# Kernel optimization log

Measured on AMD Instinct MI355X. Metric: run time of the kernel, lower is better.

## Reference

```python
import jax, jax.numpy as jnp
import numpy as np

EPS = 1e-6
N = 512
D = 8192


def solve_lap_np(cost):
    """Jonker-Volgenant shortest-augmenting-path LAP (same optimum as
    scipy.optimize.linear_sum_assignment). Returns col4row: col assigned to each row."""
    cost = np.asarray(cost, dtype=np.float64)
    n = cost.shape[0]
    u = np.zeros(n)
    v = np.zeros(n)
    path = np.full(n, -1, dtype=np.int64)
    col4row = np.full(n, -1, dtype=np.int64)
    row4col = np.full(n, -1, dtype=np.int64)
    for cur_row in range(n):
        shortest = np.full(n, np.inf)
        SR = np.zeros(n, dtype=bool)  # visited rows
        SC = np.zeros(n, dtype=bool)  # visited cols
        i = cur_row
        min_val = 0.0
        sink = -1
        while sink == -1:
            SR[i] = True
            idx = np.nonzero(~SC)[0]
            r = min_val + cost[i, idx] - u[i] - v[idx]
            upd = r < shortest[idx]
            shortest[idx[upd]] = r[upd]
            path[idx[upd]] = i
            j = idx[np.argmin(shortest[idx])]
            min_val = shortest[j]
            SC[j] = True
            if row4col[j] == -1:
                sink = j
            else:
                i = row4col[j]
        # dual updates
        u[cur_row] += min_val
        sr = np.nonzero(SR)[0]
        sr = sr[sr != cur_row]
        u[sr] += min_val - shortest[col4row[sr]]
        sc = np.nonzero(SC)[0]
        v[sc] -= min_val - shortest[sc]
        # augment along the alternating path
        j = sink
        while True:
            i = path[j]
            row4col[j] = i
            col4row[i], j = j, col4row[i]
            if i == cur_row:
                break
    return col4row


def lap_assign(cost):
    """Optimal assignment as a one-hot labelling matrix (rows -> cols)."""
    n = cost.shape[0]
    col = jax.pure_callback(
        lambda c: solve_lap_np(np.asarray(c)).astype(np.int32),
        jax.ShapeDtypeStruct((n,), jnp.int32),
        cost,
    )
    return jax.nn.one_hot(col, n, dtype=cost.dtype)


def l2_normalize(x):
    # torch F.normalize(p=2, dim=1): x / max(||x||, eps)
    norm = jnp.sqrt(jnp.sum(x * x, axis=1, keepdims=True))
    return x / jnp.maximum(norm, EPS)


def setup_inputs() -> dict:
    key = jax.random.key(0)
    k1, k2, k3 = jax.random.split(key, 3)
    return {
        "un1": jax.random.normal(k1, (N, D), dtype=jnp.float32),
        "un2": jax.random.normal(k2, (N, D), dtype=jnp.float32),
        "un3": jax.random.normal(k3, (N, D), dtype=jnp.float32),
    }


def reference(un1, un2, un3):
    n1 = l2_normalize(un1)
    n2 = l2_normalize(un2)
    n3 = l2_normalize(un3)
    # cosine-distance cost matrices, cycle 1->2->3->1
    c12 = 1.0 - n1 @ n2.T
    c23 = 1.0 - n2 @ n3.T
    c31 = 1.0 - n3 @ n1.T
    x12 = lap_assign(c12)
    x23 = lap_assign(c23)
    x31 = lap_assign(c31)
    return (x12, x23, x31)
```

## Files before the change

kernel.cpp:

```cpp
#include <hip/hip_runtime.h>
#include <math.h>

#define NN 512
#define DD 8192

__global__ __launch_bounds__(256) void norm_kernel(
    const float* __restrict__ a0, const float* __restrict__ a1,
    const float* __restrict__ a2, float* __restrict__ scales) {
  const float* mats[3] = {a0, a1, a2};
  const int m = blockIdx.y;
  const int row = blockIdx.x;
  const float* x = mats[m] + (size_t)row * DD;
  const int tid = threadIdx.x;
  float s = 0.f;
  for (int k = tid * 4; k < DD; k += 256 * 4) {
    const float4 v = *(const float4*)(x + k);
    s += v.x * v.x + v.y * v.y + v.z * v.z + v.w * v.w;
  }
#pragma unroll
  for (int off = 32; off > 0; off >>= 1) s += __shfl_down(s, off);
  __shared__ float ws[4];
  if ((tid & 63) == 0) ws[tid >> 6] = s;
  __syncthreads();
  if (tid == 0) {
    const float t = ws[0] + ws[1] + ws[2] + ws[3];
    scales[m * NN + row] = 1.0f / fmaxf(sqrtf(t), 1e-6f);
  }
}

__global__ __launch_bounds__(256) void cost_gemm_kernel(
    const float* __restrict__ a0, const float* __restrict__ a1,
    const float* __restrict__ a2, const float* __restrict__ scales,
    float* __restrict__ cost_all) {
  const float* mats[3] = {a0, a1, a2};
  const int p = blockIdx.z;
  const int pA = p, pB = (p + 1) % 3;
  const float* A = mats[pA];
  const float* B = mats[pB];
  float* C = cost_all + (size_t)p * NN * NN;

  __shared__ float lds_a[32 * 64];
  __shared__ float lds_b[32 * 64];

  const int tid = threadIdx.x;
  const int rowBase = blockIdx.y * 64;
  const int colBase = blockIdx.x * 64;

  const int lr = tid & 63;
  const int lq = tid >> 6;

  const float* Arow = A + (size_t)(rowBase + lr) * DD;
  const float* Brow = B + (size_t)(colBase + lr) * DD;

  float acc[4][4];
#pragma unroll
  for (int i = 0; i < 4; ++i)
#pragma unroll
    for (int j = 0; j < 4; ++j) acc[i][j] = 0.f;

  const int tx = tid & 15, ty = tid >> 4;

  for (int kb = 0; kb < DD; kb += 32) {
#pragma unroll
    for (int qq = 0; qq < 2; ++qq) {
      const int q = lq + qq * 4;
      const float4 av = *(const float4*)(Arow + kb + q * 4);
      const float4 bv = *(const float4*)(Brow + kb + q * 4);
      lds_a[(q * 4 + 0) * 64 + lr] = av.x;
      lds_a[(q * 4 + 1) * 64 + lr] = av.y;
      lds_a[(q * 4 + 2) * 64 + lr] = av.z;
      lds_a[(q * 4 + 3) * 64 + lr] = av.w;
      lds_b[(q * 4 + 0) * 64 + lr] = bv.x;
      lds_b[(q * 4 + 1) * 64 + lr] = bv.y;
      lds_b[(q * 4 + 2) * 64 + lr] = bv.z;
      lds_b[(q * 4 + 3) * 64 + lr] = bv.w;
    }
    __syncthreads();
#pragma unroll
    for (int k = 0; k < 32; ++k) {
      const float4 a4 = *(const float4*)(&lds_a[k * 64 + ty * 4]);
      const float4 b4 = *(const float4*)(&lds_b[k * 64 + tx * 4]);
      const float as0[4] = {a4.x, a4.y, a4.z, a4.w};
      const float bs0[4] = {b4.x, b4.y, b4.z, b4.w};
#pragma unroll
      for (int ii = 0; ii < 4; ++ii)
#pragma unroll
        for (int jj = 0; jj < 4; ++jj)
          acc[ii][jj] = fmaf(as0[ii], bs0[jj], acc[ii][jj]);
    }
    __syncthreads();
  }

#pragma unroll
  for (int ii = 0; ii < 4; ++ii) {
    const int gr = rowBase + ty * 4 + ii;
    const float sa = scales[pA * NN + gr];
#pragma unroll
    for (int jj = 0; jj < 4; ++jj) {
      const int gc = colBase + tx * 4 + jj;
      const float sb = scales[pB * NN + gc];
      C[gr * NN + gc] = 1.0f - acc[ii][jj] * sa * sb;
    }
  }
}


__device__ __forceinline__ int SW(int c) { return ((c & 7) << 6) | (c >> 3); }

__device__ __forceinline__ unsigned wave_min_u32(unsigned x) {
  int t;
  t = __builtin_amdgcn_update_dpp((int)x, (int)x, 0x111, 0xf, 0xf, false);
  x = ((unsigned)t < x) ? (unsigned)t : x;
  t = __builtin_amdgcn_update_dpp((int)x, (int)x, 0x112, 0xf, 0xf, false);
  x = ((unsigned)t < x) ? (unsigned)t : x;
  t = __builtin_amdgcn_update_dpp((int)x, (int)x, 0x114, 0xf, 0xf, false);
  x = ((unsigned)t < x) ? (unsigned)t : x;
  t = __builtin_amdgcn_update_dpp((int)x, (int)x, 0x118, 0xf, 0xf, false);
  x = ((unsigned)t < x) ? (unsigned)t : x;
  t = __builtin_amdgcn_update_dpp((int)x, (int)x, 0x142, 0xf, 0xf, false);
  x = ((unsigned)t < x) ? (unsigned)t : x;
  t = __builtin_amdgcn_update_dpp((int)x, (int)x, 0x143, 0xf, 0xf, false);
  x = ((unsigned)t < x) ? (unsigned)t : x;
  return (unsigned)__builtin_amdgcn_readlane((int)x, 63);
}

__device__ __forceinline__ double readlane_f64(double x, int lane) {
  const long long b = __double_as_longlong(x);
  const int lo = __builtin_amdgcn_readlane((int)(b & 0xffffffffLL), lane);
  const int hi = __builtin_amdgcn_readlane((int)(b >> 32), lane);
  return __longlong_as_double(((long long)hi << 32) | (unsigned long long)(unsigned)lo);
}

__global__ __launch_bounds__(64) void lap_kernel(
    const float* __restrict__ cost_all, float* __restrict__ out) {
  const int p = blockIdx.x;
  const float* cost = cost_all + (size_t)p * NN * NN;
  float* outp = out + (size_t)p * NN * NN;
  const int tid = threadIdx.x;

  __shared__ double sh_u[NN];
  __shared__ double sh_shortest[NN];
  __shared__ int sh_path[NN];
  __shared__ int sh_col4row[NN];
  __shared__ int sh_row4col[NN];

  const double INF = __builtin_inf();

  for (int k = tid; k < NN; k += 64) {
    sh_u[k] = 0.0;
    sh_col4row[k] = -1;
    sh_row4col[k] = -1;
  }
  double myV[8];
#pragma unroll
  for (int q = 0; q < 8; ++q) myV[q] = 0.0;
  __syncthreads();

  for (int cur_row = 0; cur_row < NN; ++cur_row) {
    double selv[8];
    double vAdj[8];
    double frz[8];
    int myPath[8];
    unsigned pl[8];
#pragma unroll
    for (int q = 0; q < 8; ++q) {
      selv[q] = INF;
      vAdj[q] = myV[q];
      frz[q] = 0.0;
      myPath[q] = 0;
    }
#pragma unroll
    for (int q = 0; q < 8; ++q)
      pl[q] = ((unsigned)q << 10) | (unsigned)(sh_row4col[SW(tid * 8 + q)] + 1);

    unsigned scMask = 0, srMask = 0;
    int i = cur_row;
    double minv = 0.0;
    int sink = -1;
    int pendQ = -1, pendLane = 0;

    while (true) {
      if ((i >> 3) == tid) srMask |= 1u << (i & 7);
      const float4 c0 = *(const float4*)(cost + (size_t)i * NN + tid * 8);
      const float4 c1 = *(const float4*)(cost + (size_t)i * NN + tid * 8 + 4);
      const double u_i = sh_u[SW(i)];
      if (pendQ >= 0) {
        const bool me = (tid == pendLane);
#define APPLY_SC(K)                                                     \
        if (pendQ == K) {                                               \
          if (me) {                                                     \
            selv[K] = INF; vAdj[K] = -INF; frz[K] = minv;               \
            scMask |= 1u << K;                                          \
          }                                                             \
        }
        APPLY_SC(0) APPLY_SC(1) APPLY_SC(2) APPLY_SC(3)
        APPLY_SC(4) APPLY_SC(5) APPLY_SC(6) APPLY_SC(7)
#undef APPLY_SC
      }
      const float cf[8] = {c0.x, c0.y, c0.z, c0.w, c1.x, c1.y, c1.z, c1.w};
#pragma unroll
      for (int q = 0; q < 8; ++q) {
        const double r = ((minv + (double)cf[q]) - u_i) - vAdj[q];
        const bool cnd = r < selv[q];
        selv[q] = fmin(selv[q], r);
        myPath[q] = cnd ? i : myPath[q];
      }
      const bool t01 = selv[1] < selv[0];
      double v01 = t01 ? selv[1] : selv[0]; unsigned p01 = t01 ? pl[1] : pl[0];
      const bool t23 = selv[3] < selv[2];
      double v23 = t23 ? selv[3] : selv[2]; unsigned p23 = t23 ? pl[3] : pl[2];
      const bool t45 = selv[5] < selv[4];
      double v45 = t45 ? selv[5] : selv[4]; unsigned p45 = t45 ? pl[5] : pl[4];
      const bool t67 = selv[7] < selv[6];
      double v67 = t67 ? selv[7] : selv[6]; unsigned p67 = t67 ? pl[7] : pl[6];
      const bool ta = v23 < v01;
      const double vab = ta ? v23 : v01; const unsigned pab = ta ? p23 : p01;
      const bool tb = v67 < v45;
      const double vcd = tb ? v67 : v45; const unsigned pcd = tb ? p67 : p45;
      const bool tc = vcd < vab;
      const double lv = tc ? vcd : vab; const unsigned lp = tc ? pcd : pab;
      const long long bb = __double_as_longlong(lv);
      const unsigned long long kk =
          (bb < 0) ? ~(unsigned long long)bb
                   : ((unsigned long long)bb | 0x8000000000000000ULL);
      const unsigned hi = (unsigned)(kk >> 32);
      const unsigned lo = (unsigned)kk;
      const unsigned minhi = wave_min_u32(hi);
      unsigned long long bal = __ballot(hi == minhi);
      int srcLane;
      if (__popcll(bal) == 1) {
        srcLane = __ffsll(bal) - 1;
      } else {
        const unsigned lo2 = (hi == minhi) ? lo : 0xFFFFFFFFu;
        const unsigned minlo = wave_min_u32(lo2);
        bal = __ballot((hi == minhi) && (lo == minlo));
        srcLane = __ffsll(bal) - 1;
      }
      minv = readlane_f64(lv, srcLane);
      const unsigned pw = (unsigned)__builtin_amdgcn_readlane((int)lp, srcLane);
      const int qb = (int)(pw >> 10);
      const int r4 = (int)(pw & 0x3FFu) - 1;
      if (r4 < 0) {
        sink = srcLane * 8 + qb;
        break;
      }
      i = r4;
      pendQ = qb;
      pendLane = srcLane;
    }

#pragma unroll
    for (int q = 0; q < 8; ++q) {
      sh_shortest[SW(tid * 8 + q)] = frz[q];
      sh_path[SW(tid * 8 + q)] = myPath[q];
    }
    __syncthreads();
#pragma unroll
    for (int q = 0; q < 8; ++q) {
      const int row = tid * 8 + q;
      if (row == cur_row) {
        sh_u[SW(row)] += minv;
      } else if (srMask & (1u << q)) {
        sh_u[SW(row)] += minv - sh_shortest[SW(sh_col4row[SW(row)])];
      }
      if (scMask & (1u << q)) myV[q] -= minv - frz[q];
    }
    __syncthreads();
    if (tid == 0) {
      int j = sink;
      while (true) {
        const int pi = sh_path[SW(j)];
        sh_row4col[SW(j)] = pi;
        const int tmp = sh_col4row[SW(pi)];
        sh_col4row[SW(pi)] = j;
        j = tmp;
        if (pi == cur_row) break;
      }
    }
    __syncthreads();
  }

#pragma unroll
  for (int q = 0; q < 8; ++q) {
    const int row = tid * 8 + q;
    outp[(size_t)row * NN + sh_col4row[SW(row)]] = 1.0f;
  }
}

extern "C" void kernel_launch(void* const* d_in, const int* in_sizes, int n_in,
                              void* d_out, int out_size, void* d_ws, size_t ws_size,
                              hipStream_t stream) {
  const float* un1 = (const float*)d_in[0];
  const float* un2 = (const float*)d_in[1];
  const float* un3 = (const float*)d_in[2];
  float* out = (float*)d_out;

  float* cost = (float*)d_ws;
  float* scales = cost + (size_t)3 * NN * NN;

  hipMemsetAsync(d_out, 0, (size_t)out_size * sizeof(float), stream);

  norm_kernel<<<dim3(NN, 3), 256, 0, stream>>>(un1, un2, un3, scales);
  cost_gemm_kernel<<<dim3(NN / 64, NN / 64, 3), 256, 0, stream>>>(un1, un2, un3, scales, cost);
  lap_kernel<<<3, 64, 0, stream>>>(cost, out);
}
```

Before: 5.735 ms.

## Add JV column reduction, reduction transfer and augmenting row reduction before LAP

Adds the Jonker-Volgenant initialization phases (column reduction, reduction transfer, two passes of augmenting row reduction) so that most rows are assigned before the shortest-augmenting-path phase. The augmentation loop then runs only over the remaining free rows, with a guard on the Dijkstra loop. This is meant to cut the number of expensive serial augmentations that dominate the single-wave LAP kernel. The risk is that ties may give a different optimal assignment than the reference, and the extra serial work in the preprocessing phases adds cost.

```diff
diff --git a/kernel.cpp b/kernel.cpp
--- a/kernel.cpp
+++ b/kernel.cpp
@@ -131,6 +131,30 @@
   return __longlong_as_double(((long long)hi << 32) | (unsigned long long)(unsigned)lo);
 }
 
+__device__ __forceinline__ unsigned long long f64key(double x) {
+  const long long b = __double_as_longlong(x);
+  return (b < 0) ? ~(unsigned long long)b
+                 : ((unsigned long long)b | 0x8000000000000000ULL);
+}
+
+__device__ __forceinline__ int wave_argmin_f64(double x, double* mv) {
+  const unsigned long long k = f64key(x);
+  const unsigned hi = (unsigned)(k >> 32), lo = (unsigned)k;
+  const unsigned minhi = wave_min_u32(hi);
+  unsigned long long bal = __ballot(hi == minhi);
+  int lane;
+  if (__popcll(bal) == 1) {
+    lane = __ffsll(bal) - 1;
+  } else {
+    const unsigned lo2 = (hi == minhi) ? lo : 0xFFFFFFFFu;
+    const unsigned minlo = wave_min_u32(lo2);
+    bal = __ballot((hi == minhi) && (lo == minlo));
+    lane = __ffsll(bal) - 1;
+  }
+  *mv = readlane_f64(x, lane);
+  return lane;
+}
+
 __global__ __launch_bounds__(64) void lap_kernel(
     const float* __restrict__ cost_all, float* __restrict__ out) {
   const int p = blockIdx.x;
@@ -139,24 +163,170 @@
   const int tid = threadIdx.x;
 
   __shared__ double sh_u[NN];
+  __shared__ double sh_v[NN];
   __shared__ double sh_shortest[NN];
   __shared__ int sh_path[NN];
-  __shared__ int sh_col4row[NN];
-  __shared__ int sh_row4col[NN];
+  __shared__ int sh_x[NN];
+  __shared__ int sh_y[NN];
+  __shared__ int sh_cnt[NN];
+  __shared__ int sh_free[NN];
 
   const double INF = __builtin_inf();
 
-  for (int k = tid; k < NN; k += 64) {
-    sh_u[k] = 0.0;
-    sh_col4row[k] = -1;
-    sh_row4col[k] = -1;
-  }
+#pragma unroll
+  for (int q = 0; q < 8; ++q) {
+    const int e = tid * 8 + q;
+    sh_x[SW(e)] = -1;
+    sh_y[SW(e)] = -1;
+    sh_cnt[SW(e)] = 0;
+  }
+  __syncthreads();
+
+  float colv[8];
+  int imin[8];
+#pragma unroll
+  for (int q = 0; q < 8; ++q) { colv[q] = __builtin_inff(); imin[q] = 0; }
+  for (int i = 0; i < NN; i += 2) {
+    const float4 a0 = *(const float4*)(cost + (size_t)i * NN + tid * 8);
+    const float4 a1 = *(const float4*)(cost + (size_t)i * NN + tid * 8 + 4);
+    const float4 b0 = *(const float4*)(cost + (size_t)(i + 1) * NN + tid * 8);
+    const float4 b1 = *(const float4*)(cost + (size_t)(i + 1) * NN + tid * 8 + 4);
+    const float fa[8] = {a0.x, a0.y, a0.z, a0.w, a1.x, a1.y, a1.z, a1.w};
+    const float fb[8] = {b0.x, b0.y, b0.z, b0.w, b1.x, b1.y, b1.z, b1.w};
+#pragma unroll
+    for (int q = 0; q < 8; ++q) {
+      if (fa[q] < colv[q]) { colv[q] = fa[q]; imin[q] = i; }
+      if (fb[q] < colv[q]) { colv[q] = fb[q]; imin[q] = i + 1; }
+    }
+  }
+#pragma unroll
+  for (int q = 0; q < 8; ++q) {
+    sh_v[SW(tid * 8 + q)] = (double)colv[q];
+    atomicMax(&sh_x[SW(imin[q])], tid * 8 + q);
+    atomicAdd(&sh_cnt[SW(imin[q])], 1);
+  }
+  __syncthreads();
+#pragma unroll
+  for (int q = 0; q < 8; ++q) {
+    const int j = tid * 8 + q;
+    sh_y[SW(j)] = (sh_x[SW(imin[q])] == j) ? imin[q] : -1;
+  }
+  __syncthreads();
+
+  for (int q0 = 0; q0 < 8; ++q0) {
+    const bool rt = (sh_cnt[SW(tid * 8 + q0)] == 1);
+    unsigned long long mask = __ballot(rt);
+    while (mask) {
+      const int lane = __ffsll(mask) - 1;
+      mask &= mask - 1;
+      const int i = lane * 8 + q0;
+      const int j1 = sh_x[SW(i)];
+      const float4 c0 = *(const float4*)(cost + (size_t)i * NN + tid * 8);
+      const float4 c1 = *(const float4*)(cost + (size_t)i * NN + tid * 8 + 4);
+      const float cf[8] = {c0.x, c0.y, c0.z, c0.w, c1.x, c1.y, c1.z, c1.w};
+      double m = INF;
+#pragma unroll
+      for (int q = 0; q < 8; ++q) {
+        const int col = tid * 8 + q;
+        double h = (double)cf[q] - sh_v[SW(col)];
+        if (col == j1) h = INF;
+        m = fmin(m, h);
+      }
+      double gmin;
+      (void)wave_argmin_f64(m, &gmin);
+      if (tid == 0) sh_v[SW(j1)] = sh_v[SW(j1)] - gmin;
+    }
+  }
+  __syncthreads();
+
+  int numfree = 0;
+  for (int q0 = 0; q0 < 8; ++q0) {
+    const int row = tid * 8 + q0;
+    const bool fr = (sh_x[SW(row)] < 0);
+    const unsigned long long mask = __ballot(fr);
+    if (fr) {
+      const int pos = numfree + (int)__popcll(mask & ((1ull << tid) - 1ull));
+      sh_free[pos] = row;
+    }
+    numfree += (int)__popcll(mask);
+  }
+  __syncthreads();
+
+  int nf = numfree;
+  for (int pass = 0; pass < 2; ++pass) {
+    int k = 0;
+    const int prv = nf;
+    nf = 0;
+    int guard = 0;
+    while (k < prv && ++guard < 5000) {
+      const int i = sh_free[k];
+      k++;
+      const float4 c0 = *(const float4*)(cost + (size_t)i * NN + tid * 8);
+      const float4 c1 = *(const float4*)(cost + (size_t)i * NN + tid * 8 + 4);
+      const float cf[8] = {c0.x, c0.y, c0.z, c0.w, c1.x, c1.y, c1.z, c1.w};
+      double um = (double)cf[0] - sh_v[SW(tid * 8)];
+      int j1q = tid * 8;
+      double us = INF;
+      int j2q = tid * 8;
+#pragma unroll
+      for (int q = 1; q < 8; ++q) {
+        const double h = (double)cf[q] - sh_v[SW(tid * 8 + q)];
+        const int col = tid * 8 + q;
+        if (h < us) {
+          if (h >= um) { us = h; j2q = col; }
+          else { us = um; j2q = j1q; um = h; j1q = col; }
+        }
+      }
+      double g_umin;
+      const int lane1 = wave_argmin_f64(um, &g_umin);
+      const double su = (tid == lane1) ? us : um;
+      double g_usub;
+      const int lane2 = wave_argmin_f64(su, &g_usub);
+      int j1 = __builtin_amdgcn_readlane(j1q, lane1);
+      const int j2 = __builtin_amdgcn_readlane((lane2 == lane1) ? j2q : j1q, lane2);
+      int i0 = sh_y[SW(j1)];
+      const bool strict = g_umin < g_usub;
+      if (strict) {
+        if (tid == 0) sh_v[SW(j1)] = sh_v[SW(j1)] - (g_usub - g_umin);
+      } else if (i0 >= 0) {
+        j1 = j2;
+        i0 = sh_y[SW(j1)];
+      }
+      if (tid == 0) { sh_x[SW(i)] = j1; sh_y[SW(j1)] = i; }
+      if (i0 >= 0) {
+        if (strict) {
+          k--;
+          if (tid == 0) sh_free[k] = i0;
+        } else {
+          if (tid == 0) sh_free[nf] = i0;
+          nf++;
+        }
+      }
+    }
+    if (k < prv) {
+      for (int t = k; t < prv; ++t) {
+        if (tid == 0) sh_free[nf] = sh_free[t];
+        nf++;
+      }
+    }
+  }
+  __syncthreads();
+
   double myV[8];
 #pragma unroll
-  for (int q = 0; q < 8; ++q) myV[q] = 0.0;
-  __syncthreads();
-
-  for (int cur_row = 0; cur_row < NN; ++cur_row) {
+  for (int q = 0; q < 8; ++q) {
+    const int row = tid * 8 + q;
+    const int xr = sh_x[SW(row)];
+    double uu = 0.0;
+    if (xr >= 0) uu = (double)cost[(size_t)row * NN + xr] - sh_v[SW(xr)];
+    sh_u[SW(row)] = uu;
+    myV[q] = sh_v[SW(tid * 8 + q)];
+  }
+  __syncthreads();
+
+  for (int ff = 0; ff < nf; ++ff) {
+    const int cur_row = sh_free[ff];
+
     double selv[8];
     double vAdj[8];
     double frz[8];
@@ -171,15 +341,16 @@
     }
 #pragma unroll
     for (int q = 0; q < 8; ++q)
-      pl[q] = ((unsigned)q << 10) | (unsigned)(sh_row4col[SW(tid * 8 + q)] + 1);
+      pl[q] = ((unsigned)q << 10) | (unsigned)(sh_y[SW(tid * 8 + q)] + 1);
 
     unsigned scMask = 0, srMask = 0;
     int i = cur_row;
     double minv = 0.0;
     int sink = -1;
     int pendQ = -1, pendLane = 0;
-
-    while (true) {
+    int guard = 0;
+
+    while (++guard <= NN + 2) {
       if ((i >> 3) == tid) srMask |= 1u << (i & 7);
       const float4 c0 = *(const float4*)(cost + (size_t)i * NN + tid * 8);
       const float4 c1 = *(const float4*)(cost + (size_t)i * NN + tid * 8 + 4);
@@ -219,10 +390,7 @@
       const double vcd = tb ? v67 : v45; const unsigned pcd = tb ? p67 : p45;
       const bool tc = vcd < vab;
       const double lv = tc ? vcd : vab; const unsigned lp = tc ? pcd : pab;
-      const long long bb = __double_as_longlong(lv);
-      const unsigned long long kk =
-          (bb < 0) ? ~(unsigned long long)bb
-                   : ((unsigned long long)bb | 0x8000000000000000ULL);
+      const unsigned long long kk = f64key(lv);
       const unsigned hi = (unsigned)(kk >> 32);
       const unsigned lo = (unsigned)kk;
       const unsigned minhi = wave_min_u32(hi);
@@ -249,41 +417,43 @@
       pendLane = srcLane;
     }
 
-#pragma unroll
-    for (int q = 0; q < 8; ++q) {
-      sh_shortest[SW(tid * 8 + q)] = frz[q];
-      sh_path[SW(tid * 8 + q)] = myPath[q];
-    }
-    __syncthreads();
-#pragma unroll
-    for (int q = 0; q < 8; ++q) {
-      const int row = tid * 8 + q;
-      if (row == cur_row) {
-        sh_u[SW(row)] += minv;
-      } else if (srMask & (1u << q)) {
-        sh_u[SW(row)] += minv - sh_shortest[SW(sh_col4row[SW(row)])];
-      }
-      if (scMask & (1u << q)) myV[q] -= minv - frz[q];
-    }
-    __syncthreads();
-    if (tid == 0) {
-      int j = sink;
-      while (true) {
-        const int pi = sh_path[SW(j)];
-        sh_row4col[SW(j)] = pi;
-        const int tmp = sh_col4row[SW(pi)];
-        sh_col4row[SW(pi)] = j;
-        j = tmp;
-        if (pi == cur_row) break;
-      }
-    }
-    __syncthreads();
+    if (sink >= 0) {
+#pragma unroll
+      for (int q = 0; q < 8; ++q) {
+        sh_shortest[SW(tid * 8 + q)] = frz[q];
+        sh_path[SW(tid * 8 + q)] = myPath[q];
+      }
+      __syncthreads();
+#pragma unroll
+      for (int q = 0; q < 8; ++q) {
+        const int row = tid * 8 + q;
+        if (row == cur_row) {
+          sh_u[SW(row)] += minv;
+        } else if (srMask & (1u << q)) {
+          sh_u[SW(row)] += minv - sh_shortest[SW(sh_x[SW(row)])];
+        }
+        if (scMask & (1u << q)) myV[q] -= minv - frz[q];
+      }
+      __syncthreads();
+      if (tid == 0) {
+        int j = sink;
+        while (true) {
+          const int pi = sh_path[SW(j)];
+          sh_y[SW(j)] = pi;
+          const int tmp = sh_x[SW(pi)];
+          sh_x[SW(pi)] = j;
+          j = tmp;
+          if (pi == cur_row) break;
+        }
+      }
+      __syncthreads();
+    }
   }
 
 #pragma unroll
   for (int q = 0; q < 8; ++q) {
     const int row = tid * 8 + q;
-    outp[(size_t)row * NN + sh_col4row[SW(row)]] = 1.0f;
+    outp[(size_t)row * NN + sh_x[SW(row)]] = 1.0f;
   }
 }
 
```

Result: slower. 11.27 ms (+96.5%).

## Add JV column-reduction initialization to LAP so augmentation runs only for free rows

Applied to the files above, without the earlier changes.

Adds a Jonker-Volgenant style column reduction before augmentation. Each column's dual is set to its minimum cost, that minimum row is assigned when uncontested, and the free rows are compacted into a list so the shortest-augmenting-path phase only iterates over unassigned rows. It also precomputes minv-u_i-v per column to trim the inner double-precision arithmetic, and adds a loop guard. This aims to cut the number of serial Dijkstra augmentations, at the cost of a full cost-matrix scan and a risk of ties or degenerate cases yielding a different optimal assignment.

```diff
diff --git a/kernel.cpp b/kernel.cpp
--- a/kernel.cpp
+++ b/kernel.cpp
@@ -131,6 +131,12 @@
   return __longlong_as_double(((long long)hi << 32) | (unsigned long long)(unsigned)lo);
 }
 
+__device__ __forceinline__ unsigned long long f64key(double x) {
+  const long long b = __double_as_longlong(x);
+  return (b < 0) ? ~(unsigned long long)b
+                 : ((unsigned long long)b | 0x8000000000000000ULL);
+}
+
 __global__ __launch_bounds__(64) void lap_kernel(
     const float* __restrict__ cost_all, float* __restrict__ out) {
   const int p = blockIdx.x;
@@ -141,22 +147,67 @@
   __shared__ double sh_u[NN];
   __shared__ double sh_shortest[NN];
   __shared__ int sh_path[NN];
-  __shared__ int sh_col4row[NN];
-  __shared__ int sh_row4col[NN];
+  __shared__ int sh_x[NN];
+  __shared__ int sh_y[NN];
+  __shared__ int sh_free[NN];
 
   const double INF = __builtin_inf();
 
-  for (int k = tid; k < NN; k += 64) {
-    sh_u[k] = 0.0;
-    sh_col4row[k] = -1;
-    sh_row4col[k] = -1;
+#pragma unroll
+  for (int q = 0; q < 8; ++q) {
+    const int e = tid * 8 + q;
+    sh_x[SW(e)] = -1;
+    sh_y[SW(e)] = -1;
+    sh_u[SW(e)] = 0.0;
+  }
+  __syncthreads();
+
+  float colv[8];
+  int imin[8];
+#pragma unroll
+  for (int q = 0; q < 8; ++q) { colv[q] = __builtin_inff(); imin[q] = 0; }
+  for (int i = 0; i < NN; i += 2) {
+    const float4 a0 = *(const float4*)(cost + (size_t)i * NN + tid * 8);
+    const float4 a1 = *(const float4*)(cost + (size_t)i * NN + tid * 8 + 4);
+    const float4 b0 = *(const float4*)(cost + (size_t)(i + 1) * NN + tid * 8);
+    const float4 b1 = *(const float4*)(cost + (size_t)(i + 1) * NN + tid * 8 + 4);
+    const float fa[8] = {a0.x, a0.y, a0.z, a0.w, a1.x, a1.y, a1.z, a1.w};
+    const float fb[8] = {b0.x, b0.y, b0.z, b0.w, b1.x, b1.y, b1.z, b1.w};
+#pragma unroll
+    for (int q = 0; q < 8; ++q) {
+      if (fa[q] < colv[q]) { colv[q] = fa[q]; imin[q] = i; }
+      if (fb[q] < colv[q]) { colv[q] = fb[q]; imin[q] = i + 1; }
+    }
+  }
+#pragma unroll
+  for (int q = 0; q < 8; ++q) atomicMax(&sh_x[SW(imin[q])], tid * 8 + q);
+  __syncthreads();
+#pragma unroll
+  for (int q = 0; q < 8; ++q) {
+    const int j = tid * 8 + q;
+    sh_y[SW(j)] = (sh_x[SW(imin[q])] == j) ? imin[q] : -1;
   }
   double myV[8];
 #pragma unroll
-  for (int q = 0; q < 8; ++q) myV[q] = 0.0;
-  __syncthreads();
-
-  for (int cur_row = 0; cur_row < NN; ++cur_row) {
+  for (int q = 0; q < 8; ++q) myV[q] = (double)colv[q];
+  __syncthreads();
+
+  int numfree = 0;
+  for (int q0 = 0; q0 < 8; ++q0) {
+    const int row = tid * 8 + q0;
+    const bool fr = (sh_x[SW(row)] < 0);
+    const unsigned long long mask = __ballot(fr);
+    if (fr) {
+      const int pos = numfree + (int)__popcll(mask & ((1ull << tid) - 1ull));
+      sh_free[pos] = row;
+    }
+    numfree += (int)__popcll(mask);
+  }
+  __syncthreads();
+
+  for (int ff = 0; ff < numfree; ++ff) {
+    const int cur_row = sh_free[ff];
+
     double selv[8];
     double vAdj[8];
     double frz[8];
@@ -171,15 +222,16 @@
     }
 #pragma unroll
     for (int q = 0; q < 8; ++q)
-      pl[q] = ((unsigned)q << 10) | (unsigned)(sh_row4col[SW(tid * 8 + q)] + 1);
+      pl[q] = ((unsigned)q << 10) | (unsigned)(sh_y[SW(tid * 8 + q)] + 1);
 
     unsigned scMask = 0, srMask = 0;
     int i = cur_row;
     double minv = 0.0;
     int sink = -1;
     int pendQ = -1, pendLane = 0;
-
-    while (true) {
+    int guard = 0;
+
+    while (++guard <= NN + 2) {
       if ((i >> 3) == tid) srMask |= 1u << (i & 7);
       const float4 c0 = *(const float4*)(cost + (size_t)i * NN + tid * 8);
       const float4 c1 = *(const float4*)(cost + (size_t)i * NN + tid * 8 + 4);
@@ -197,10 +249,14 @@
         APPLY_SC(4) APPLY_SC(5) APPLY_SC(6) APPLY_SC(7)
 #undef APPLY_SC
       }
+      const double mu = minv - u_i;
+      double base[8];
+#pragma unroll
+      for (int q = 0; q < 8; ++q) base[q] = mu - vAdj[q];
       const float cf[8] = {c0.x, c0.y, c0.z, c0.w, c1.x, c1.y, c1.z, c1.w};
 #pragma unroll
       for (int q = 0; q < 8; ++q) {
-        const double r = ((minv + (double)cf[q]) - u_i) - vAdj[q];
+        const double r = (double)cf[q] + base[q];
         const bool cnd = r < selv[q];
         selv[q] = fmin(selv[q], r);
         myPath[q] = cnd ? i : myPath[q];
@@ -219,10 +275,7 @@
       const double vcd = tb ? v67 : v45; const unsigned pcd = tb ? p67 : p45;
       const bool tc = vcd < vab;
       const double lv = tc ? vcd : vab; const unsigned lp = tc ? pcd : pab;
-      const long long bb = __double_as_longlong(lv);
-      const unsigned long long kk =
-          (bb < 0) ? ~(unsigned long long)bb
-                   : ((unsigned long long)bb | 0x8000000000000000ULL);
+      const unsigned long long kk = f64key(lv);
       const unsigned hi = (unsigned)(kk >> 32);
       const unsigned lo = (unsigned)kk;
       const unsigned minhi = wave_min_u32(hi);
@@ -249,41 +302,44 @@
       pendLane = srcLane;
     }
 
-#pragma unroll
-    for (int q = 0; q < 8; ++q) {
-      sh_shortest[SW(tid * 8 + q)] = frz[q];
-      sh_path[SW(tid * 8 + q)] = myPath[q];
-    }
-    __syncthreads();
-#pragma unroll
-    for (int q = 0; q < 8; ++q) {
-      const int row = tid * 8 + q;
-      if (row == cur_row) {
-        sh_u[SW(row)] += minv;
-      } else if (srMask & (1u << q)) {
-        sh_u[SW(row)] += minv - sh_shortest[SW(sh_col4row[SW(row)])];
-      }
-      if (scMask & (1u << q)) myV[q] -= minv - frz[q];
-    }
-    __syncthreads();
-    if (tid == 0) {
-      int j = sink;
-      while (true) {
-        const int pi = sh_path[SW(j)];
-        sh_row4col[SW(j)] = pi;
-        const int tmp = sh_col4row[SW(pi)];
-        sh_col4row[SW(pi)] = j;
-        j = tmp;
-        if (pi == cur_row) break;
-      }
-    }
-    __syncthreads();
+    if (sink >= 0) {
+#pragma unroll
+      for (int q = 0; q < 8; ++q) {
+        sh_shortest[SW(tid * 8 + q)] = frz[q];
+        sh_path[SW(tid * 8 + q)] = myPath[q];
+      }
+      __syncthreads();
+#pragma unroll
+      for (int q = 0; q < 8; ++q) {
+        const int row = tid * 8 + q;
+        if (row == cur_row) {
+          sh_u[SW(row)] += minv;
+        } else if (srMask & (1u << q)) {
+          sh_u[SW(row)] += minv - sh_shortest[SW(sh_x[SW(row)])];
+        }
+        if (scMask & (1u << q)) myV[q] -= minv - frz[q];
+      }
+      __syncthreads();
+      if (tid == 0) {
+        int j = sink;
+        while (true) {
+          const int pi = sh_path[SW(j)];
+          sh_y[SW(j)] = pi;
+          const int tmp = sh_x[SW(pi)];
+          sh_x[SW(pi)] = j;
+          j = tmp;
+          if (pi == cur_row) break;
+        }
+      }
+      __syncthreads();
+    }
   }
 
 #pragma unroll
   for (int q = 0; q < 8; ++q) {
     const int row = tid * 8 + q;
-    outp[(size_t)row * NN + sh_col4row[SW(row)]] = 1.0f;
+    const int xc = sh_x[SW(row)];
+    if (xc >= 0) outp[(size_t)row * NN + xc] = 1.0f;
   }
 }
 
```

After: 6.080 ms. +6.0%, slower.
